# Kernel optimization log

Hardware: AMD Instinct MI355X
Metric: run time of the kernel (lower is better)

## Reference

```python
import jax, jax.numpy as jnp
import numpy as np

N_NODES = 40000
N_EDGES = 1280000
D_FEAT = 1024
HIDDEN = 64
N_CLASSES = 40


def gcn_conv(x, edge_index, W, b):
    # PyG GCNConv: linear transform, add self-loops, symmetric deg^{-1/2} normalization, scatter-add
    n = x.shape[0]
    h = x @ W  # [N, out]
    loop = jnp.arange(n, dtype=edge_index.dtype)
    row = jnp.concatenate([edge_index[0], loop])  # source
    col = jnp.concatenate([edge_index[1], loop])  # target
    deg = jax.ops.segment_sum(jnp.ones_like(col, dtype=x.dtype), col, num_segments=n)
    dinv = jnp.where(deg > 0, jax.lax.rsqrt(deg), 0.0).astype(x.dtype)
    norm = dinv[row] * dinv[col]  # [E+N]
    msg = h[row] * norm[:, None]
    out = jax.ops.segment_sum(msg, col, num_segments=n)
    return out + b


def setup_inputs() -> dict:
    key = jax.random.key(0)
    k1, k2, k3, k4 = jax.random.split(key, 4)
    x = jax.random.normal(k1, (N_NODES, D_FEAT), dtype=jnp.float32)
    edge_index = jax.random.randint(k2, (2, N_EDGES), 0, N_NODES, dtype=jnp.int32)
    W1 = jax.random.normal(k3, (D_FEAT, HIDDEN), dtype=jnp.float32) * (1.0 / np.sqrt(D_FEAT))
    b1 = jnp.zeros((HIDDEN,), dtype=jnp.float32)
    W2 = jax.random.normal(k4, (HIDDEN, N_CLASSES), dtype=jnp.float32) * (1.0 / np.sqrt(HIDDEN))
    b2 = jnp.zeros((N_CLASSES,), dtype=jnp.float32)
    return {"x": x, "edge_index": edge_index, "W1": W1, "b1": b1, "W2": W2, "b2": b2}


def reference(x, edge_index, W1, b1, W2, b2):
    h = gcn_conv(x, edge_index, W1, b1)
    h = jax.nn.relu(h)
    # F.dropout(training=False) -> identity in eval mode
    h = gcn_conv(h, edge_index, W2, b2)
    return jax.nn.log_softmax(h, axis=1)
```

## Files before the change

kernel.cpp:

```cpp
#include <hip/hip_runtime.h>
#include <hip/hip_bf16.h>
#include <math.h>

#define N_NODES 40000
#define N_EDGES 1280000
#define D_FEAT 1024
#define HIDDEN 64
#define N_CLASSES 40
#define NB 157
#define CHUNK 4096

typedef _Float16 f16x8 __attribute__((ext_vector_type(8)));
typedef float f32x4 __attribute__((ext_vector_type(4)));


#define HIST_BLOCKS 313
#define CONV_BLOCKS 256

__global__ __launch_bounds__(256) void k_pre(const int* __restrict__ col,
                                             int* __restrict__ btot,
                                             const float* __restrict__ W,
                                             _Float16* __restrict__ Wt) {
    __shared__ int h[NB];
    int tid = threadIdx.x;
    if (blockIdx.x < HIST_BLOCKS) {
        if (tid < NB) h[tid] = 0;
        __syncthreads();
        int e0 = blockIdx.x * 4096;
        int e1 = min(e0 + 4096, N_EDGES);
        for (int e = e0 + tid; e < e1; e += 256)
            atomicAdd(&h[col[e] >> 8], 1);
        __syncthreads();
        if (tid < NB && h[tid]) atomicAdd(&btot[tid], h[tid]);
    } else {
        int i = (blockIdx.x - HIST_BLOCKS) * 256 + tid;
        int n = i & 63, k = i >> 6;
        Wt[n * D_FEAT + k] = (_Float16)W[k * HIDDEN + n];
    }
}


__global__ __launch_bounds__(256) void k_binscatter(const int* __restrict__ row,
                                                    const int* __restrict__ col,
                                                    const int* __restrict__ btot,
                                                    int* __restrict__ gcur,
                                                    unsigned* __restrict__ sedge) {
    __shared__ unsigned stage[CHUNK];
    __shared__ unsigned char bo[CHUNK];
    __shared__ int sc[256];
    __shared__ int bb[NB];
    __shared__ int hist[NB];
    __shared__ int lo[NB];
    __shared__ int cur[NB];
    __shared__ int dst[NB];
    const int tid = threadIdx.x;
    const int e0 = blockIdx.x * CHUNK;
    const int nE = min(CHUNK, N_EDGES - e0);

    if (tid < NB) { hist[tid] = 0; cur[tid] = 0; }
    int bv = (tid < NB) ? btot[tid] : 0;
    sc[tid] = bv;
    __syncthreads();
#pragma unroll
    for (int d = 1; d < 256; d <<= 1) {
        int t = (tid >= d) ? sc[tid - d] : 0;
        __syncthreads();
        sc[tid] += t;
        __syncthreads();
    }
    if (tid < NB) bb[tid] = sc[tid] - bv;

    int c[16];
#pragma unroll
    for (int t = 0; t < 16; ++t) {
        int e = tid + t * 256;
        c[t] = (e < nE) ? col[e0 + e] : -1;
        if (e < nE) atomicAdd(&hist[c[t] >> 8], 1);
    }
    __syncthreads();

    int hv = (tid < NB) ? hist[tid] : 0;
    sc[tid] = hv;
    __syncthreads();
#pragma unroll
    for (int d = 1; d < 256; d <<= 1) {
        int t = (tid >= d) ? sc[tid - d] : 0;
        __syncthreads();
        sc[tid] += t;
        __syncthreads();
    }
    if (tid < NB) {
        int excl = sc[tid] - hv;
        lo[tid] = excl;
        int cp = hv ? atomicAdd(&gcur[tid], hv) : 0;
        dst[tid] = bb[tid] + cp - excl;
    }
    __syncthreads();

#pragma unroll
    for (int t = 0; t < 16; ++t) {
        int e = tid + t * 256;
        if (e < nE) {
            int b = c[t] >> 8;
            int p = lo[b] + atomicAdd(&cur[b], 1);
            stage[p] = ((unsigned)(c[t] & 255) << 16) | (unsigned)row[e0 + e];
            bo[p] = (unsigned char)b;
        }
    }
    __syncthreads();
    for (int i = tid; i < nE; i += 256)
        sedge[dst[bo[i]] + i] = stage[i];
}


__global__ __launch_bounds__(256) void k_bucketsort(const unsigned* __restrict__ sedge,
                                                    const int* __restrict__ btot,
                                                    int* __restrict__ off,
                                                    float* __restrict__ dinv,
                                                    unsigned short* __restrict__ sorted) {
    __shared__ int sc[256];
    __shared__ int hist[256];
    __shared__ int cur[256];
    const int tid = threadIdx.x;
    const int b = blockIdx.x;
    int bv = (tid < NB) ? btot[tid] : 0;
    sc[tid] = bv;
    hist[tid] = 0;
    __syncthreads();
#pragma unroll
    for (int d = 1; d < 256; d <<= 1) {
        int t = (tid >= d) ? sc[tid - d] : 0;
        __syncthreads();
        sc[tid] += t;
        __syncthreads();
    }
    const int base = (b == 0) ? 0 : sc[b - 1];
    const int end  = sc[b];
    __syncthreads();

    for (int i = base + tid; i < end; i += 256)
        atomicAdd(&hist[sedge[i] >> 16], 1);
    __syncthreads();
    int v = hist[tid];
    sc[tid] = v;
    __syncthreads();
#pragma unroll
    for (int d = 1; d < 256; d <<= 1) {
        int t = (tid >= d) ? sc[tid - d] : 0;
        __syncthreads();
        sc[tid] += t;
        __syncthreads();
    }
    int excl = sc[tid] - v;
    cur[tid] = excl;
    int col0 = b << 8;
    int ncol = min(256, N_NODES - col0);
    if (tid < ncol) {
        off[col0 + tid] = base + excl;
        dinv[col0 + tid] = rsqrtf((float)(v + 1));
    }
    if (b == NB - 1 && tid == 0) off[N_NODES] = N_EDGES;
    __syncthreads();
    for (int i = base + tid; i < end; i += 256) {
        unsigned e = sedge[i];
        int p = atomicAdd(&cur[e >> 16], 1);
        sorted[base + p] = (unsigned short)e;
    }
}


#define LDA 72
#define LDB 72

__global__ __launch_bounds__(256) void k_gemm1(const float* __restrict__ X,
                                               const _Float16* __restrict__ Wt,
                                               const float* __restrict__ dinv,
                                               _Float16* __restrict__ out) {
    __shared__ _Float16 As[32 * LDA];
    __shared__ _Float16 Bs[64 * LDB];
    const int tid = threadIdx.x;
    const int wave = tid >> 6, lane = tid & 63;
    const int row0 = blockIdx.x * 32;
    const int m0 = (wave & 1) * 16, n0 = (wave >> 1) * 32;
    const int lr = lane & 15, quad = lane >> 4;

    const int ar = tid >> 3;
    const int ak = (tid & 7) * 8;
    const int bn = tid >> 2;
    const int bk = (tid & 3) * 16;

    f32x4 acc0 = {0.f,0.f,0.f,0.f}, acc1 = {0.f,0.f,0.f,0.f};

    for (int k0 = 0; k0 < D_FEAT; k0 += 64) {
        const float* xp = &X[(row0 + ar) * D_FEAT + k0 + ak];
        float4 v0 = *(const float4*)(xp + 0);
        float4 v1 = *(const float4*)(xp + 4);
        f16x8 p0 = {(_Float16)v0.x,(_Float16)v0.y,(_Float16)v0.z,(_Float16)v0.w,
                    (_Float16)v1.x,(_Float16)v1.y,(_Float16)v1.z,(_Float16)v1.w};
        *(f16x8*)&As[ar * LDA + ak] = p0;
        const uint4* wp = (const uint4*)&Wt[bn * D_FEAT + k0 + bk];
        uint4 w0 = wp[0], w1 = wp[1];
        *(uint4*)&Bs[bn * LDB + bk]     = w0;
        *(uint4*)&Bs[bn * LDB + bk + 8] = w1;
        __syncthreads();
#pragma unroll
        for (int kk = 0; kk < 64; kk += 32) {
            f16x8 a  = *(f16x8*)&As[(m0 + lr) * LDA + kk + quad * 8];
            f16x8 b0 = *(f16x8*)&Bs[(n0 + lr) * LDB + kk + quad * 8];
            f16x8 b1 = *(f16x8*)&Bs[(n0 + 16 + lr) * LDB + kk + quad * 8];
            acc0 = __builtin_amdgcn_mfma_f32_16x16x32_f16(a, b0, acc0, 0, 0, 0);
            acc1 = __builtin_amdgcn_mfma_f32_16x16x32_f16(a, b1, acc1, 0, 0, 0);
        }
        __syncthreads();
    }

#pragma unroll
    for (int r = 0; r < 4; ++r) {
        int m = row0 + m0 + quad * 4 + r;
        float dv = dinv[m];
        out[m * HIDDEN + n0 + lr]      = (_Float16)(acc0[r] * dv);
        out[m * HIDDEN + n0 + 16 + lr] = (_Float16)(acc1[r] * dv);
    }
}


__global__ __launch_bounds__(256) void k_agg1(const int* __restrict__ off,
                                              const unsigned short* __restrict__ sorted,
                                              const _Float16* __restrict__ hs,
                                              const float* __restrict__ dinv,
                                              const float* __restrict__ bias,
                                              _Float16* __restrict__ A1) {
    const int tid = threadIdx.x;
    const int wave = tid >> 6, lane = tid & 63;
    const int node = blockIdx.x * 4 + wave;
    const int g = lane >> 3;
    const int sl = lane & 7;

    float acc[8];
#pragma unroll
    for (int j = 0; j < 8; ++j) acc[j] = 0.f;
    if (g == 0) {
        f16x8 v = *(const f16x8*)&hs[node * HIDDEN + sl * 8];
#pragma unroll
        for (int j = 0; j < 8; ++j) acc[j] = (float)v[j];
    }

    const int beg = off[node], end = off[node + 1];
    for (int base = beg; base < end; base += 64) {
        int m = end - base; if (m > 64) m = 64;
        int vidx = (lane < m) ? (int)sorted[base + lane] : 0;
        int nfull = m & ~15;
        int i = 0;
        for (; i < nfull; i += 16) {
            int s0 = __shfl(vidx, i + g, 64);
            int s1 = __shfl(vidx, i + 8 + g, 64);
            f16x8 v0 = *(const f16x8*)&hs[s0 * HIDDEN + sl * 8];
            f16x8 v1 = *(const f16x8*)&hs[s1 * HIDDEN + sl * 8];
#pragma unroll
            for (int j = 0; j < 8; ++j)
                acc[j] += (float)v0[j] + (float)v1[j];
        }
        if (i < m) {
            int s0 = __shfl(vidx, i + g, 64);
            int s1 = __shfl(vidx, i + 8 + g, 64);
            f16x8 v0 = {};
            f16x8 v1 = {};
            if (i + g < m)     v0 = *(const f16x8*)&hs[s0 * HIDDEN + sl * 8];
            if (i + 8 + g < m) v1 = *(const f16x8*)&hs[s1 * HIDDEN + sl * 8];
#pragma unroll
            for (int j = 0; j < 8; ++j)
                acc[j] += (float)v0[j] + (float)v1[j];
        }
    }

#pragma unroll
    for (int j = 0; j < 8; ++j) {
        acc[j] += __shfl_xor(acc[j], 8, 64);
        acc[j] += __shfl_xor(acc[j], 16, 64);
        acc[j] += __shfl_xor(acc[j], 32, 64);
    }
    if (lane < 8) {
        float dv = dinv[node];
        f16x8 o;
#pragma unroll
        for (int j = 0; j < 8; ++j) {
            float z = fmaf(dv, acc[j], bias[lane * 8 + j]);
            o[j] = (_Float16)(fmaxf(z, 0.f) * dv);
        }
        *(f16x8*)&A1[node * HIDDEN + lane * 8] = o;
    }
}


__global__ __launch_bounds__(256) void k_agg2_lsm(const int* __restrict__ off,
                                                  const unsigned short* __restrict__ sorted,
                                                  const _Float16* __restrict__ A1,
                                                  const float* __restrict__ dinv,
                                                  const float* __restrict__ b2,
                                                  const float* __restrict__ W2,
                                                  float* __restrict__ out) {
    __shared__ float W2s[HIDDEN * N_CLASSES];
    __shared__ float aggs[4][HIDDEN];
    const int tid = threadIdx.x;
    for (int i = tid; i < HIDDEN * N_CLASSES; i += 256) W2s[i] = W2[i];
    const int wave = tid >> 6, lane = tid & 63;
    const int node = blockIdx.x * 4 + wave;
    const int g = lane >> 3, sl = lane & 7;

    float acc[8];
#pragma unroll
    for (int j = 0; j < 8; ++j) acc[j] = 0.f;
    if (g == 0) {
        f16x8 v = *(const f16x8*)&A1[node * HIDDEN + sl * 8];
#pragma unroll
        for (int j = 0; j < 8; ++j) acc[j] = (float)v[j];
    }
    __syncthreads();

    const int beg = off[node], end = off[node + 1];
    for (int base = beg; base < end; base += 64) {
        int m = end - base; if (m > 64) m = 64;
        int vidx = (lane < m) ? (int)sorted[base + lane] : 0;
        int nfull = m & ~15;
        int i = 0;
        for (; i < nfull; i += 16) {
            int s0 = __shfl(vidx, i + g, 64);
            int s1 = __shfl(vidx, i + 8 + g, 64);
            f16x8 v0 = *(const f16x8*)&A1[s0 * HIDDEN + sl * 8];
            f16x8 v1 = *(const f16x8*)&A1[s1 * HIDDEN + sl * 8];
#pragma unroll
            for (int j = 0; j < 8; ++j)
                acc[j] += (float)v0[j] + (float)v1[j];
        }
        if (i < m) {
            int s0 = __shfl(vidx, i + g, 64);
            int s1 = __shfl(vidx, i + 8 + g, 64);
            f16x8 v0 = {};
            f16x8 v1 = {};
            if (i + g < m)     v0 = *(const f16x8*)&A1[s0 * HIDDEN + sl * 8];
            if (i + 8 + g < m) v1 = *(const f16x8*)&A1[s1 * HIDDEN + sl * 8];
#pragma unroll
            for (int j = 0; j < 8; ++j)
                acc[j] += (float)v0[j] + (float)v1[j];
        }
    }
#pragma unroll
    for (int j = 0; j < 8; ++j) {
        acc[j] += __shfl_xor(acc[j], 8, 64);
        acc[j] += __shfl_xor(acc[j], 16, 64);
        acc[j] += __shfl_xor(acc[j], 32, 64);
    }
    if (lane < 8) {
        f32x4 t0 = {acc[0], acc[1], acc[2], acc[3]};
        f32x4 t1 = {acc[4], acc[5], acc[6], acc[7]};
        *(f32x4*)&aggs[wave][lane * 8]     = t0;
        *(f32x4*)&aggs[wave][lane * 8 + 4] = t1;
    }
    __builtin_amdgcn_wave_barrier();

    float z = -INFINITY;
    if (lane < N_CLASSES) {
        float s = 0.f;
        const float* ag = aggs[wave];
#pragma unroll
        for (int k = 0; k < HIDDEN; ++k)
            s = fmaf(ag[k], W2s[k * N_CLASSES + lane], s);
        z = fmaf(dinv[node], s, b2[lane]);
    }
    float mv = z;
#pragma unroll
    for (int d = 32; d > 0; d >>= 1) mv = fmaxf(mv, __shfl_xor(mv, d, 64));
    float ex = (lane < N_CLASSES) ? expf(z - mv) : 0.f;
#pragma unroll
    for (int d = 32; d > 0; d >>= 1) ex += __shfl_xor(ex, d, 64);
    float lse = mv + logf(ex);
    if (lane < N_CLASSES) out[node * N_CLASSES + lane] = z - lse;
}


extern "C" void kernel_launch(void* const* d_in, const int* in_sizes, int n_in,
                              void* d_out, int out_size, void* d_ws, size_t ws_size,
                              hipStream_t stream) {
    const float* x  = (const float*)d_in[0];
    const int*   ei = (const int*)d_in[1];
    const float* W1 = (const float*)d_in[2];
    const float* b1 = (const float*)d_in[3];
    const float* W2 = (const float*)d_in[4];
    const float* b2 = (const float*)d_in[5];
    const int* row = ei;
    const int* col = ei + N_EDGES;

    char* ws = (char*)d_ws;
    int*            btot   = (int*)(ws + 0);
    int*            gcur   = (int*)(ws + 1024);
    int*            off    = (int*)(ws + 4096);
    float*          dinv   = (float*)(ws + 167936);
    unsigned*       sedge  = (unsigned*)(ws + 335872);
    unsigned short* sorted = (unsigned short*)(ws + 5455872);
    _Float16*       W1t    = (_Float16*)(ws + 8015872);
    _Float16*       B1     = (_Float16*)(ws + 8146944);
    _Float16*       A1     = (_Float16*)(ws + 335872);

    hipMemsetAsync(btot, 0, 2048, stream);
    k_pre<<<HIST_BLOCKS + CONV_BLOCKS, 256, 0, stream>>>(col, btot, W1, W1t);
    k_binscatter<<<(N_EDGES + CHUNK - 1) / CHUNK, 256, 0, stream>>>(row, col, btot, gcur, sedge);
    k_bucketsort<<<NB, 256, 0, stream>>>(sedge, btot, off, dinv, sorted);

    k_gemm1<<<N_NODES / 32, 256, 0, stream>>>(x, W1t, dinv, B1);
    k_agg1<<<N_NODES / 4, 256, 0, stream>>>(off, sorted, B1, dinv, b1, A1);
    k_agg2_lsm<<<N_NODES / 4, 256, 0, stream>>>(off, sorted, A1, dinv, b2, W2, (float*)d_out);
}
```

Measured before the change: 384.5 us.

## Replace two-pass bucket sort with atomic degree count, scan, and scatter CSR build

Rebuilds the CSR construction: a per-node atomic degree histogram, a three-kernel prefix scan, then an atomic-position scatter of source indices. This replaces the two-level bin scatter and bucket sort. The GEMM now streams X with nontemporal loads, and the aggregation loops add the two f16 neighbor vectors in half precision before converting to fp32. The new scatter leaves edge order within each node nondeterministic, which affects float summation order, and the f16 pair add slightly lowers precision. It also adds kernel launches and heavy global atomics, in exchange for fewer passes over the edge list.

```diff
diff --git a/kernel.cpp b/kernel.cpp
--- a/kernel.cpp
+++ b/kernel.cpp
@@ -8,58 +8,41 @@
 #define HIDDEN 64
 #define N_CLASSES 40
 #define NB 157
-#define CHUNK 4096
 
 typedef _Float16 f16x8 __attribute__((ext_vector_type(8)));
 typedef float f32x4 __attribute__((ext_vector_type(4)));
 
 
-#define HIST_BLOCKS 313
-#define CONV_BLOCKS 256
-
-__global__ __launch_bounds__(256) void k_pre(const int* __restrict__ col,
-                                             int* __restrict__ btot,
-                                             const float* __restrict__ W,
-                                             _Float16* __restrict__ Wt) {
-    __shared__ int h[NB];
-    int tid = threadIdx.x;
-    if (blockIdx.x < HIST_BLOCKS) {
-        if (tid < NB) h[tid] = 0;
-        __syncthreads();
-        int e0 = blockIdx.x * 4096;
-        int e1 = min(e0 + 4096, N_EDGES);
-        for (int e = e0 + tid; e < e1; e += 256)
-            atomicAdd(&h[col[e] >> 8], 1);
-        __syncthreads();
-        if (tid < NB && h[tid]) atomicAdd(&btot[tid], h[tid]);
+#define EDGE_BLOCKS 1250
+
+__global__ __launch_bounds__(256) void k_preA(const int* __restrict__ col,
+                                              int* __restrict__ deg,
+                                              const float* __restrict__ W,
+                                              _Float16* __restrict__ Wt) {
+    const int tid = threadIdx.x;
+    if (blockIdx.x < EDGE_BLOCKS) {
+        int e0 = blockIdx.x * 1024 + tid * 4;
+        int4 c = *(const int4*)&col[e0];
+        atomicAdd(&deg[c.x], 1);
+        atomicAdd(&deg[c.y], 1);
+        atomicAdd(&deg[c.z], 1);
+        atomicAdd(&deg[c.w], 1);
     } else {
-        int i = (blockIdx.x - HIST_BLOCKS) * 256 + tid;
+        int i = (blockIdx.x - EDGE_BLOCKS) * 256 + tid;
         int n = i & 63, k = i >> 6;
         Wt[n * D_FEAT + k] = (_Float16)W[k * HIDDEN + n];
     }
 }
 
 
-__global__ __launch_bounds__(256) void k_binscatter(const int* __restrict__ row,
-                                                    const int* __restrict__ col,
-                                                    const int* __restrict__ btot,
-                                                    int* __restrict__ gcur,
-                                                    unsigned* __restrict__ sedge) {
-    __shared__ unsigned stage[CHUNK];
-    __shared__ unsigned char bo[CHUNK];
+__global__ __launch_bounds__(256) void k_scanA(const int* __restrict__ deg,
+                                               int* __restrict__ lsum,
+                                               int* __restrict__ bsum) {
     __shared__ int sc[256];
-    __shared__ int bb[NB];
-    __shared__ int hist[NB];
-    __shared__ int lo[NB];
-    __shared__ int cur[NB];
-    __shared__ int dst[NB];
-    const int tid = threadIdx.x;
-    const int e0 = blockIdx.x * CHUNK;
-    const int nE = min(CHUNK, N_EDGES - e0);
-
-    if (tid < NB) { hist[tid] = 0; cur[tid] = 0; }
-    int bv = (tid < NB) ? btot[tid] : 0;
-    sc[tid] = bv;
+    const int tid = threadIdx.x;
+    const int i = blockIdx.x * 256 + tid;
+    int v = (i < N_NODES) ? deg[i] : 0;
+    sc[tid] = v;
     __syncthreads();
 #pragma unroll
     for (int d = 1; d < 256; d <<= 1) {
@@ -68,19 +51,16 @@
         sc[tid] += t;
         __syncthreads();
     }
-    if (tid < NB) bb[tid] = sc[tid] - bv;
-
-    int c[16];
-#pragma unroll
-    for (int t = 0; t < 16; ++t) {
-        int e = tid + t * 256;
-        c[t] = (e < nE) ? col[e0 + e] : -1;
-        if (e < nE) atomicAdd(&hist[c[t] >> 8], 1);
-    }
-    __syncthreads();
-
-    int hv = (tid < NB) ? hist[tid] : 0;
-    sc[tid] = hv;
+    if (i < N_NODES) lsum[i] = sc[tid] - v;
+    if (tid == 255) bsum[blockIdx.x] = sc[255];
+}
+
+__global__ __launch_bounds__(256) void k_scanB(const int* __restrict__ bsum,
+                                               int* __restrict__ bbase) {
+    __shared__ int sc[256];
+    const int tid = threadIdx.x;
+    int v = (tid < NB) ? bsum[tid] : 0;
+    sc[tid] = v;
     __syncthreads();
 #pragma unroll
     for (int d = 1; d < 256; d <<= 1) {
@@ -89,83 +69,37 @@
         sc[tid] += t;
         __syncthreads();
     }
-    if (tid < NB) {
-        int excl = sc[tid] - hv;
-        lo[tid] = excl;
-        int cp = hv ? atomicAdd(&gcur[tid], hv) : 0;
-        dst[tid] = bb[tid] + cp - excl;
-    }
-    __syncthreads();
-
-#pragma unroll
-    for (int t = 0; t < 16; ++t) {
-        int e = tid + t * 256;
-        if (e < nE) {
-            int b = c[t] >> 8;
-            int p = lo[b] + atomicAdd(&cur[b], 1);
-            stage[p] = ((unsigned)(c[t] & 255) << 16) | (unsigned)row[e0 + e];
-            bo[p] = (unsigned char)b;
-        }
-    }
-    __syncthreads();
-    for (int i = tid; i < nE; i += 256)
-        sedge[dst[bo[i]] + i] = stage[i];
-}
-
-
-__global__ __launch_bounds__(256) void k_bucketsort(const unsigned* __restrict__ sedge,
-                                                    const int* __restrict__ btot,
-                                                    int* __restrict__ off,
-                                                    float* __restrict__ dinv,
-                                                    unsigned short* __restrict__ sorted) {
-    __shared__ int sc[256];
-    __shared__ int hist[256];
-    __shared__ int cur[256];
-    const int tid = threadIdx.x;
-    const int b = blockIdx.x;
-    int bv = (tid < NB) ? btot[tid] : 0;
-    sc[tid] = bv;
-    hist[tid] = 0;
-    __syncthreads();
-#pragma unroll
-    for (int d = 1; d < 256; d <<= 1) {
-        int t = (tid >= d) ? sc[tid - d] : 0;
-        __syncthreads();
-        sc[tid] += t;
-        __syncthreads();
-    }
-    const int base = (b == 0) ? 0 : sc[b - 1];
-    const int end  = sc[b];
-    __syncthreads();
-
-    for (int i = base + tid; i < end; i += 256)
-        atomicAdd(&hist[sedge[i] >> 16], 1);
-    __syncthreads();
-    int v = hist[tid];
-    sc[tid] = v;
-    __syncthreads();
-#pragma unroll
-    for (int d = 1; d < 256; d <<= 1) {
-        int t = (tid >= d) ? sc[tid - d] : 0;
-        __syncthreads();
-        sc[tid] += t;
-        __syncthreads();
-    }
-    int excl = sc[tid] - v;
-    cur[tid] = excl;
-    int col0 = b << 8;
-    int ncol = min(256, N_NODES - col0);
-    if (tid < ncol) {
-        off[col0 + tid] = base + excl;
-        dinv[col0 + tid] = rsqrtf((float)(v + 1));
-    }
-    if (b == NB - 1 && tid == 0) off[N_NODES] = N_EDGES;
-    __syncthreads();
-    for (int i = base + tid; i < end; i += 256) {
-        unsigned e = sedge[i];
-        int p = atomicAdd(&cur[e >> 16], 1);
-        sorted[base + p] = (unsigned short)e;
-    }
+    if (tid < NB) bbase[tid] = sc[tid] - v;
+}
+
+__global__ __launch_bounds__(256) void k_scanC(const int* __restrict__ deg,
+                                               const int* __restrict__ lsum,
+                                               const int* __restrict__ bbase,
+                                               int* __restrict__ off,
+                                               int* __restrict__ pos,
+                                               float* __restrict__ dinv) {
+    const int i = blockIdx.x * 256 + threadIdx.x;
+    if (i < N_NODES) {
+        int v = lsum[i] + bbase[blockIdx.x];
+        off[i] = v;
+        pos[i] = v;
+        dinv[i] = rsqrtf((float)(deg[i] + 1));
+    }
+    if (i == 0) off[N_NODES] = N_EDGES;
+}
+
+
+__global__ __launch_bounds__(256) void k_scatter(const int* __restrict__ row,
+                                                 const int* __restrict__ col,
+                                                 int* __restrict__ pos,
+                                                 unsigned short* __restrict__ sorted) {
+    int e0 = blockIdx.x * 1024 + threadIdx.x * 4;
+    int4 c = *(const int4*)&col[e0];
+    int4 r = *(const int4*)&row[e0];
+    int p0 = atomicAdd(&pos[c.x], 1); sorted[p0] = (unsigned short)r.x;
+    int p1 = atomicAdd(&pos[c.y], 1); sorted[p1] = (unsigned short)r.y;
+    int p2 = atomicAdd(&pos[c.z], 1); sorted[p2] = (unsigned short)r.z;
+    int p3 = atomicAdd(&pos[c.w], 1); sorted[p3] = (unsigned short)r.w;
 }
 
 
@@ -192,11 +126,11 @@
     f32x4 acc0 = {0.f,0.f,0.f,0.f}, acc1 = {0.f,0.f,0.f,0.f};
 
     for (int k0 = 0; k0 < D_FEAT; k0 += 64) {
-        const float* xp = &X[(row0 + ar) * D_FEAT + k0 + ak];
-        float4 v0 = *(const float4*)(xp + 0);
-        float4 v1 = *(const float4*)(xp + 4);
-        f16x8 p0 = {(_Float16)v0.x,(_Float16)v0.y,(_Float16)v0.z,(_Float16)v0.w,
-                    (_Float16)v1.x,(_Float16)v1.y,(_Float16)v1.z,(_Float16)v1.w};
+        const f32x4* xp = (const f32x4*)&X[(row0 + ar) * D_FEAT + k0 + ak];
+        f32x4 v0 = __builtin_nontemporal_load(xp);
+        f32x4 v1 = __builtin_nontemporal_load(xp + 1);
+        f16x8 p0 = {(_Float16)v0[0],(_Float16)v0[1],(_Float16)v0[2],(_Float16)v0[3],
+                    (_Float16)v1[0],(_Float16)v1[1],(_Float16)v1[2],(_Float16)v1[3]};
         *(f16x8*)&As[ar * LDA + ak] = p0;
         const uint4* wp = (const uint4*)&Wt[bn * D_FEAT + k0 + bk];
         uint4 w0 = wp[0], w1 = wp[1];
@@ -256,9 +190,10 @@
             int s1 = __shfl(vidx, i + 8 + g, 64);
             f16x8 v0 = *(const f16x8*)&hs[s0 * HIDDEN + sl * 8];
             f16x8 v1 = *(const f16x8*)&hs[s1 * HIDDEN + sl * 8];
+            f16x8 t = v0 + v1;
 #pragma unroll
             for (int j = 0; j < 8; ++j)
-                acc[j] += (float)v0[j] + (float)v1[j];
+                acc[j] += (float)t[j];
         }
         if (i < m) {
             int s0 = __shfl(vidx, i + g, 64);
@@ -267,9 +202,10 @@
             f16x8 v1 = {};
             if (i + g < m)     v0 = *(const f16x8*)&hs[s0 * HIDDEN + sl * 8];
             if (i + 8 + g < m) v1 = *(const f16x8*)&hs[s1 * HIDDEN + sl * 8];
+            f16x8 t = v0 + v1;
 #pragma unroll
             for (int j = 0; j < 8; ++j)
-                acc[j] += (float)v0[j] + (float)v1[j];
+                acc[j] += (float)t[j];
         }
     }
 
@@ -328,9 +264,10 @@
             int s1 = __shfl(vidx, i + 8 + g, 64);
             f16x8 v0 = *(const f16x8*)&A1[s0 * HIDDEN + sl * 8];
             f16x8 v1 = *(const f16x8*)&A1[s1 * HIDDEN + sl * 8];
+            f16x8 t = v0 + v1;
 #pragma unroll
             for (int j = 0; j < 8; ++j)
-                acc[j] += (float)v0[j] + (float)v1[j];
+                acc[j] += (float)t[j];
         }
         if (i < m) {
             int s0 = __shfl(vidx, i + g, 64);
@@ -339,9 +276,10 @@
             f16x8 v1 = {};
             if (i + g < m)     v0 = *(const f16x8*)&A1[s0 * HIDDEN + sl * 8];
             if (i + 8 + g < m) v1 = *(const f16x8*)&A1[s1 * HIDDEN + sl * 8];
+            f16x8 t = v0 + v1;
 #pragma unroll
             for (int j = 0; j < 8; ++j)
-                acc[j] += (float)v0[j] + (float)v1[j];
+                acc[j] += (float)t[j];
         }
     }
 #pragma unroll
@@ -391,20 +329,24 @@
     const int* col = ei + N_EDGES;
 
     char* ws = (char*)d_ws;
-    int*            btot   = (int*)(ws + 0);
-    int*            gcur   = (int*)(ws + 1024);
-    int*            off    = (int*)(ws + 4096);
-    float*          dinv   = (float*)(ws + 167936);
-    unsigned*       sedge  = (unsigned*)(ws + 335872);
-    unsigned short* sorted = (unsigned short*)(ws + 5455872);
-    _Float16*       W1t    = (_Float16*)(ws + 8015872);
-    _Float16*       B1     = (_Float16*)(ws + 8146944);
-    _Float16*       A1     = (_Float16*)(ws + 335872);
-
-    hipMemsetAsync(btot, 0, 2048, stream);
-    k_pre<<<HIST_BLOCKS + CONV_BLOCKS, 256, 0, stream>>>(col, btot, W1, W1t);
-    k_binscatter<<<(N_EDGES + CHUNK - 1) / CHUNK, 256, 0, stream>>>(row, col, btot, gcur, sedge);
-    k_bucketsort<<<NB, 256, 0, stream>>>(sedge, btot, off, dinv, sorted);
+    int*            deg    = (int*)(ws + 0);
+    int*            lsum   = (int*)(ws + 163840);
+    int*            bsum   = (int*)(ws + 327680);
+    int*            bbase  = (int*)(ws + 331776);
+    int*            off    = (int*)(ws + 335872);
+    int*            pos    = (int*)(ws + 499712);
+    float*          dinv   = (float*)(ws + 663552);
+    unsigned short* sorted = (unsigned short*)(ws + 827392);
+    _Float16*       W1t    = (_Float16*)(ws + 3387392);
+    _Float16*       B1     = (_Float16*)(ws + 3518464);
+    _Float16*       A1     = (_Float16*)(ws + 8638464);
+
+    hipMemsetAsync(deg, 0, N_NODES * sizeof(int), stream);
+    k_preA<<<EDGE_BLOCKS + 256, 256, 0, stream>>>(col, deg, W1, W1t);
+    k_scanA<<<NB, 256, 0, stream>>>(deg, lsum, bsum);
+    k_scanB<<<1, 256, 0, stream>>>(bsum, bbase);
+    k_scanC<<<NB, 256, 0, stream>>>(deg, lsum, bbase, off, pos, dinv);
+    k_scatter<<<EDGE_BLOCKS, 256, 0, stream>>>(row, col, pos, sorted);
 
     k_gemm1<<<N_NODES / 32, 256, 0, stream>>>(x, W1t, dinv, B1);
     k_agg1<<<N_NODES / 4, 256, 0, stream>>>(off, sorted, B1, dinv, b1, A1);
```

After: 453.7 us. 1.18x slower.

## Double-buffer GEMM1 with 64-row tiles and pair-sum gathers in fp16

Applied to the files above, without the earlier changes.

The first GEMM now uses 64-row tiles, so each wave computes a 2x2 set of MFMA tiles. It double-buffers shared memory so the global loads for the next K slice overlap with the MFMAs on the current one, and it halves the grid. Both aggregation kernels now add the two gathered fp16 vectors in fp16 before converting to fp32, which cuts conversion work but loses some accumulation precision. With the larger tiles and 625 blocks, the GEMM has fewer blocks and more registers per thread, which could lower occupancy.

```diff
diff --git a/kernel.cpp b/kernel.cpp
--- a/kernel.cpp
+++ b/kernel.cpp
@@ -176,51 +176,79 @@
                                                const _Float16* __restrict__ Wt,
                                                const float* __restrict__ dinv,
                                                _Float16* __restrict__ out) {
-    __shared__ _Float16 As[32 * LDA];
-    __shared__ _Float16 Bs[64 * LDB];
+    __shared__ _Float16 As[2][64 * LDA];
+    __shared__ _Float16 Bs[2][64 * LDB];
     const int tid = threadIdx.x;
     const int wave = tid >> 6, lane = tid & 63;
-    const int row0 = blockIdx.x * 32;
-    const int m0 = (wave & 1) * 16, n0 = (wave >> 1) * 32;
+    const int row0 = blockIdx.x * 64;
+    const int m0 = (wave & 1) * 32, n0 = (wave >> 1) * 32;
     const int lr = lane & 15, quad = lane >> 4;
 
-    const int ar = tid >> 3;
-    const int ak = (tid & 7) * 8;
+    const int ar = tid >> 2;
+    const int ak = (tid & 3) * 16;
     const int bn = tid >> 2;
     const int bk = (tid & 3) * 16;
 
-    f32x4 acc0 = {0.f,0.f,0.f,0.f}, acc1 = {0.f,0.f,0.f,0.f};
-
-    for (int k0 = 0; k0 < D_FEAT; k0 += 64) {
-        const float* xp = &X[(row0 + ar) * D_FEAT + k0 + ak];
-        float4 v0 = *(const float4*)(xp + 0);
-        float4 v1 = *(const float4*)(xp + 4);
-        f16x8 p0 = {(_Float16)v0.x,(_Float16)v0.y,(_Float16)v0.z,(_Float16)v0.w,
-                    (_Float16)v1.x,(_Float16)v1.y,(_Float16)v1.z,(_Float16)v1.w};
-        *(f16x8*)&As[ar * LDA + ak] = p0;
-        const uint4* wp = (const uint4*)&Wt[bn * D_FEAT + k0 + bk];
-        uint4 w0 = wp[0], w1 = wp[1];
-        *(uint4*)&Bs[bn * LDB + bk]     = w0;
-        *(uint4*)&Bs[bn * LDB + bk + 8] = w1;
-        __syncthreads();
-#pragma unroll
-        for (int kk = 0; kk < 64; kk += 32) {
-            f16x8 a  = *(f16x8*)&As[(m0 + lr) * LDA + kk + quad * 8];
-            f16x8 b0 = *(f16x8*)&Bs[(n0 + lr) * LDB + kk + quad * 8];
-            f16x8 b1 = *(f16x8*)&Bs[(n0 + 16 + lr) * LDB + kk + quad * 8];
-            acc0 = __builtin_amdgcn_mfma_f32_16x16x32_f16(a, b0, acc0, 0, 0, 0);
-            acc1 = __builtin_amdgcn_mfma_f32_16x16x32_f16(a, b1, acc1, 0, 0, 0);
-        }
-        __syncthreads();
-    }
+    f32x4 acc00 = {0.f,0.f,0.f,0.f}, acc01 = {0.f,0.f,0.f,0.f};
+    f32x4 acc10 = {0.f,0.f,0.f,0.f}, acc11 = {0.f,0.f,0.f,0.f};
+
+    float4 xv0, xv1, xv2, xv3;
+    uint4 wv0, wv1;
+
+#define GLOAD(K0) {                                                          \
+        const float4* xp = (const float4*)&X[(row0 + ar) * D_FEAT + (K0) + ak]; \
+        xv0 = xp[0]; xv1 = xp[1]; xv2 = xp[2]; xv3 = xp[3];                  \
+        const uint4* wp = (const uint4*)&Wt[bn * D_FEAT + (K0) + bk];        \
+        wv0 = wp[0]; wv1 = wp[1]; }
+
+#define LSTORE(B) {                                                          \
+        f16x8 p0 = {(_Float16)xv0.x,(_Float16)xv0.y,(_Float16)xv0.z,(_Float16)xv0.w, \
+                    (_Float16)xv1.x,(_Float16)xv1.y,(_Float16)xv1.z,(_Float16)xv1.w}; \
+        f16x8 p1 = {(_Float16)xv2.x,(_Float16)xv2.y,(_Float16)xv2.z,(_Float16)xv2.w, \
+                    (_Float16)xv3.x,(_Float16)xv3.y,(_Float16)xv3.z,(_Float16)xv3.w}; \
+        *(f16x8*)&As[B][ar * LDA + ak]     = p0;                             \
+        *(f16x8*)&As[B][ar * LDA + ak + 8] = p1;                             \
+        *(uint4*)&Bs[B][bn * LDB + bk]     = wv0;                            \
+        *(uint4*)&Bs[B][bn * LDB + bk + 8] = wv1; }
+
+#define MFMA_STEP(B) {                                                       \
+        _Pragma("unroll")                                                    \
+        for (int kk = 0; kk < 64; kk += 32) {                                \
+            f16x8 a0 = *(f16x8*)&As[B][(m0 + lr) * LDA + kk + quad * 8];     \
+            f16x8 a1 = *(f16x8*)&As[B][(m0 + 16 + lr) * LDA + kk + quad * 8];\
+            f16x8 b0 = *(f16x8*)&Bs[B][(n0 + lr) * LDB + kk + quad * 8];     \
+            f16x8 b1 = *(f16x8*)&Bs[B][(n0 + 16 + lr) * LDB + kk + quad * 8];\
+            acc00 = __builtin_amdgcn_mfma_f32_16x16x32_f16(a0, b0, acc00, 0, 0, 0); \
+            acc01 = __builtin_amdgcn_mfma_f32_16x16x32_f16(a0, b1, acc01, 0, 0, 0); \
+            acc10 = __builtin_amdgcn_mfma_f32_16x16x32_f16(a1, b0, acc10, 0, 0, 0); \
+            acc11 = __builtin_amdgcn_mfma_f32_16x16x32_f16(a1, b1, acc11, 0, 0, 0); \
+        } }
+
+    GLOAD(0);
+    LSTORE(0);
+    __syncthreads();
+    int buf = 0;
+    for (int k0 = 64; k0 < D_FEAT; k0 += 64) {
+        GLOAD(k0);
+        MFMA_STEP(buf);
+        LSTORE(buf ^ 1);
+        __syncthreads();
+        buf ^= 1;
+    }
+    MFMA_STEP(buf);
 
 #pragma unroll
     for (int r = 0; r < 4; ++r) {
         int m = row0 + m0 + quad * 4 + r;
-        float dv = dinv[m];
-        out[m * HIDDEN + n0 + lr]      = (_Float16)(acc0[r] * dv);
-        out[m * HIDDEN + n0 + 16 + lr] = (_Float16)(acc1[r] * dv);
-    }
+        float dv0 = dinv[m], dv1 = dinv[m + 16];
+        out[m * HIDDEN + n0 + lr]             = (_Float16)(acc00[r] * dv0);
+        out[m * HIDDEN + n0 + 16 + lr]        = (_Float16)(acc01[r] * dv0);
+        out[(m + 16) * HIDDEN + n0 + lr]      = (_Float16)(acc10[r] * dv1);
+        out[(m + 16) * HIDDEN + n0 + 16 + lr] = (_Float16)(acc11[r] * dv1);
+    }
+#undef GLOAD
+#undef LSTORE
+#undef MFMA_STEP
 }
 
 
@@ -256,9 +284,10 @@
             int s1 = __shfl(vidx, i + 8 + g, 64);
             f16x8 v0 = *(const f16x8*)&hs[s0 * HIDDEN + sl * 8];
             f16x8 v1 = *(const f16x8*)&hs[s1 * HIDDEN + sl * 8];
+            f16x8 t = v0 + v1;
 #pragma unroll
             for (int j = 0; j < 8; ++j)
-                acc[j] += (float)v0[j] + (float)v1[j];
+                acc[j] += (float)t[j];
         }
         if (i < m) {
             int s0 = __shfl(vidx, i + g, 64);
@@ -267,9 +296,10 @@
             f16x8 v1 = {};
             if (i + g < m)     v0 = *(const f16x8*)&hs[s0 * HIDDEN + sl * 8];
             if (i + 8 + g < m) v1 = *(const f16x8*)&hs[s1 * HIDDEN + sl * 8];
+            f16x8 t = v0 + v1;
 #pragma unroll
             for (int j = 0; j < 8; ++j)
-                acc[j] += (float)v0[j] + (float)v1[j];
+                acc[j] += (float)t[j];
         }
     }
 
@@ -328,9 +358,10 @@
             int s1 = __shfl(vidx, i + 8 + g, 64);
             f16x8 v0 = *(const f16x8*)&A1[s0 * HIDDEN + sl * 8];
             f16x8 v1 = *(const f16x8*)&A1[s1 * HIDDEN + sl * 8];
+            f16x8 t = v0 + v1;
 #pragma unroll
             for (int j = 0; j < 8; ++j)
-                acc[j] += (float)v0[j] + (float)v1[j];
+                acc[j] += (float)t[j];
         }
         if (i < m) {
             int s0 = __shfl(vidx, i + g, 64);
@@ -339,9 +370,10 @@
             f16x8 v1 = {};
             if (i + g < m)     v0 = *(const f16x8*)&A1[s0 * HIDDEN + sl * 8];
             if (i + 8 + g < m) v1 = *(const f16x8*)&A1[s1 * HIDDEN + sl * 8];
+            f16x8 t = v0 + v1;
 #pragma unroll
             for (int j = 0; j < 8; ++j)
-                acc[j] += (float)v0[j] + (float)v1[j];
+                acc[j] += (float)t[j];
         }
     }
 #pragma unroll
@@ -406,7 +438,7 @@
     k_binscatter<<<(N_EDGES + CHUNK - 1) / CHUNK, 256, 0, stream>>>(row, col, btot, gcur, sedge);
     k_bucketsort<<<NB, 256, 0, stream>>>(sedge, btot, off, dinv, sorted);
 
-    k_gemm1<<<N_NODES / 32, 256, 0, stream>>>(x, W1t, dinv, B1);
+    k_gemm1<<<N_NODES / 64, 256, 0, stream>>>(x, W1t, dinv, B1);
     k_agg1<<<N_NODES / 4, 256, 0, stream>>>(off, sorted, B1, dinv, b1, A1);
     k_agg2_lsm<<<N_NODES / 4, 256, 0, stream>>>(off, sorted, A1, dinv, b2, W2, (float*)d_out);
 }
```

New measurement: 382.9 us. About the same (-0.4%).
